# Performance work log

Measured on AMD Instinct MI355X. Metric: run time of the kernel, lower is better.

The kernel has to match this reference:

```python
import jax, jax.numpy as jnp
import numpy as np

B, TV, TH, F, H, D = 16, 128, 64, 512, 512, 256


def setup_inputs() -> dict:
    key = jax.random.key(0)
    ks = jax.random.split(key, 6)
    return {
        "v": jax.random.normal(ks[0], (B, TV, F), dtype=jnp.float32),
        "h": jax.random.normal(ks[1], (B, TH, H), dtype=jnp.float32),
        "W": jax.random.normal(ks[2], (F, D), dtype=jnp.float32) * 0.05,
        "U": jax.random.normal(ks[3], (H, D), dtype=jnp.float32) * 0.05,
        "b": jax.random.normal(ks[4], (D,), dtype=jnp.float32) * 0.05,
        "w": jax.random.normal(ks[5], (D, 1), dtype=jnp.float32) * 0.05,
    }


def reference(v, h, W, U, b, w):
    # v: [B, Tv, F] video features; h: [B, Th, H] decoder hidden states
    Wv = jnp.einsum("btf,fd->btd", v, W)      # [B, Tv, D]
    Uh = jnp.einsum("bsh,hd->bsd", h, U)      # [B, Th, D]
    # Broadcast add -> [B, Th, Tv, D], tanh nonlinearity (additive attention)
    f = jnp.tanh(Uh[:, :, None, :] + Wv[:, None, :, :] + b)
    q = jnp.einsum("bstd,d->bst", f, w[:, 0])  # scores [B, Th, Tv]
    beta = jax.nn.softmax(q, axis=-1)           # softmax over Tv (axis -2 of q[..., None])
    u = jnp.einsum("bst,btf->bsf", beta, v)    # context [B, Th, F]
    return u
```

## Files before the change

### kernel.cpp

```cpp
#include <hip/hip_runtime.h>
#include <hip/hip_bf16.h>

#define BB 16
#define TV 128
#define TH 64
#define FF 512
#define HH 512
#define DD 256

#define LOG2E2 2.8853900817779268f

typedef __attribute__((ext_vector_type(8))) short bf16x8;
typedef __attribute__((ext_vector_type(4))) float f32x4;

__device__ __forceinline__ float fast_exp2(float x) {
#if __has_builtin(__builtin_amdgcn_exp2f)
  return __builtin_amdgcn_exp2f(x);
#else
  return __expf(x * 0.6931471805599453f);
#endif
}
__device__ __forceinline__ float fast_rcp(float x) {
#if __has_builtin(__builtin_amdgcn_rcpf)
  return __builtin_amdgcn_rcpf(x);
#else
  return 1.0f / x;
#endif
}
__device__ __forceinline__ unsigned short f2bf(float x) {
  union { float f; unsigned u; } a; a.f = x;
  unsigned r = a.u + 0x7fffu + ((a.u >> 16) & 1u);
  return (unsigned short)(r >> 16);
}

__device__ __forceinline__ bf16x8 cvt8(const float4 x, const float4 y) {
  union { bf16x8 v; unsigned short e[8]; } r;
  r.e[0] = f2bf(x.x); r.e[1] = f2bf(x.y); r.e[2] = f2bf(x.z); r.e[3] = f2bf(x.w);
  r.e[4] = f2bf(y.x); r.e[5] = f2bf(y.y); r.e[6] = f2bf(y.z); r.e[7] = f2bf(y.w);
  return r.v;
}

__global__ __launch_bounds__(256) void convert_wu_kernel(
    const float* __restrict__ W, const float* __restrict__ U,
    unsigned short* __restrict__ WT, unsigned short* __restrict__ UT) {
  int t2 = blockIdx.x * 256 + threadIdx.x;
  const float* S;
  unsigned short* Dt;
  if (t2 < 32768) { S = W; Dt = WT; } else { S = U; Dt = UT; t2 -= 32768; }
  int n = t2 & 255, k4 = t2 >> 8;
  float a0 = S[(k4 * 4 + 0) * 256 + n];
  float a1 = S[(k4 * 4 + 1) * 256 + n];
  float a2 = S[(k4 * 4 + 2) * 256 + n];
  float a3 = S[(k4 * 4 + 3) * 256 + n];
  ushort4 o = make_ushort4(f2bf(a0), f2bf(a1), f2bf(a2), f2bf(a3));
  *(ushort4*)&Dt[(size_t)n * 512 + k4 * 4] = o;
}

__global__ __launch_bounds__(64) void mfma_gemm_kernel(
    const float* __restrict__ Av, const float* __restrict__ Ah,
    const unsigned short* __restrict__ WT, const unsigned short* __restrict__ UT,
    const float* __restrict__ bias, float* __restrict__ EaT,
    float* __restrict__ EuhT) {
  const int bid = blockIdx.x;
  const float* A;
  const unsigned short* BT;
  int mt, nt;
  bool is_wv;
  if (bid < 256) {
    A = Av; BT = WT; is_wv = true;
    mt = bid >> 2; nt = bid & 3;
  } else {
    const int b2 = bid - 256;
    A = Ah; BT = UT; is_wv = false;
    mt = b2 >> 2; nt = b2 & 3;
  }
  const int lane = threadIdx.x & 63;
  const int m0   = mt * 32;
  const int n0   = nt * 64;
  const int r16  = lane & 15;
  const int quad = lane >> 4;

  const float* a0p = A + (size_t)(m0 + r16) * 512 + quad * 8;
  const float* a1p = a0p + 16 * 512;
  const unsigned short* bp0 = BT + (size_t)(n0 + r16) * 512 + quad * 8;
  const unsigned short* bp1 = bp0 + 16 * 512;
  const unsigned short* bp2 = bp0 + 32 * 512;
  const unsigned short* bp3 = bp0 + 48 * 512;

  f32x4 acc[2][4];
#pragma unroll
  for (int i = 0; i < 2; i++)
#pragma unroll
    for (int j = 0; j < 4; j++) acc[i][j] = (f32x4){0.f, 0.f, 0.f, 0.f};

#pragma unroll
  for (int kc = 0; kc < 16; kc++) {
    float4 a0lo = *(const float4*)(a0p + kc * 32);
    float4 a0hi = *(const float4*)(a0p + kc * 32 + 4);
    float4 a1lo = *(const float4*)(a1p + kc * 32);
    float4 a1hi = *(const float4*)(a1p + kc * 32 + 4);
    bf16x8 fa0 = cvt8(a0lo, a0hi);
    bf16x8 fa1 = cvt8(a1lo, a1hi);
    bf16x8 fb0 = *(const bf16x8*)(bp0 + kc * 32);
    bf16x8 fb1 = *(const bf16x8*)(bp1 + kc * 32);
    bf16x8 fb2 = *(const bf16x8*)(bp2 + kc * 32);
    bf16x8 fb3 = *(const bf16x8*)(bp3 + kc * 32);
    acc[0][0] = __builtin_amdgcn_mfma_f32_16x16x32_bf16(fa0, fb0, acc[0][0], 0, 0, 0);
    acc[0][1] = __builtin_amdgcn_mfma_f32_16x16x32_bf16(fa0, fb1, acc[0][1], 0, 0, 0);
    acc[0][2] = __builtin_amdgcn_mfma_f32_16x16x32_bf16(fa0, fb2, acc[0][2], 0, 0, 0);
    acc[0][3] = __builtin_amdgcn_mfma_f32_16x16x32_bf16(fa0, fb3, acc[0][3], 0, 0, 0);
    acc[1][0] = __builtin_amdgcn_mfma_f32_16x16x32_bf16(fa1, fb0, acc[1][0], 0, 0, 0);
    acc[1][1] = __builtin_amdgcn_mfma_f32_16x16x32_bf16(fa1, fb1, acc[1][1], 0, 0, 0);
    acc[1][2] = __builtin_amdgcn_mfma_f32_16x16x32_bf16(fa1, fb2, acc[1][2], 0, 0, 0);
    acc[1][3] = __builtin_amdgcn_mfma_f32_16x16x32_bf16(fa1, fb3, acc[1][3], 0, 0, 0);
  }

  if (is_wv) {
    const int bb = m0 >> 7;
    const int tb = (m0 & 127) + quad * 4;
    float* Wb = EaT + (size_t)bb * 32768;
#pragma unroll
    for (int i = 0; i < 2; i++) {
#pragma unroll
      for (int j = 0; j < 4; j++) {
#pragma unroll
        for (int r = 0; r < 4; r++) {
          Wb[(size_t)(n0 + 16 * j + r16) * 128 + tb + 16 * i + r] =
              fast_exp2(acc[i][j][r] * LOG2E2);
        }
      }
    }
  } else {
    float bj[4];
#pragma unroll
    for (int j = 0; j < 4; j++) bj[j] = bias[n0 + 16 * j + r16];
#pragma unroll
    for (int i = 0; i < 2; i++) {
#pragma unroll
      for (int j = 0; j < 4; j++) {
#pragma unroll
        for (int r = 0; r < 4; r++) {
          const int row = m0 + 16 * i + quad * 4 + r;
          EuhT[(size_t)row * 256 + n0 + 16 * j + r16] =
              fast_exp2((acc[i][j][r] + bj[j]) * LOG2E2);
        }
      }
    }
  }
}

__global__ __launch_bounds__(1024) void attn_fused_kernel(
    const float* __restrict__ EaT, const float* __restrict__ EuhT,
    const float* __restrict__ wg, const float* __restrict__ v,
    float* __restrict__ u) {
  __shared__ float EuhS[4 * 256];
  __shared__ float wS[256];
  __shared__ float pS[4 * 16 * 128];
  __shared__ float bS[4 * 128];
  __shared__ float mW[8];
  __shared__ float sW[8];

  const int tid = threadIdx.x;
  const int bid  = blockIdx.x;
  const int slot = bid >> 3;
  const int b    = (bid & 7) * 2 + (slot >> 4);
  const int sg   = slot & 15;
  const int s0   = sg * 4;

  if (tid < 256) {
    const int row = tid >> 6, q4 = (tid & 63) << 2;
    *(float4*)&EuhS[row * 256 + q4] =
        *(const float4*)&EuhT[(size_t)(b * 64 + s0 + row) * 256 + q4];
  } else if (tid < 320) {
    const int q4 = (tid - 256) << 2;
    *(float4*)&wS[q4] = *(const float4*)&wg[q4];
  }
  __syncthreads();

  {
    const int t4  = tid & 31;
    const int dgf = tid >> 5;
    const float* eab = EaT + (size_t)b * 32768 + (size_t)dgf * 8 * 128 + t4 * 4;

    float eu[4][8];
    float wr[8];
#pragma unroll
    for (int s = 0; s < 4; s++) {
      *(float4*)&eu[s][0] = *(const float4*)&EuhS[s * 256 + dgf * 8];
      *(float4*)&eu[s][4] = *(const float4*)&EuhS[s * 256 + dgf * 8 + 4];
    }
    *(float4*)&wr[0] = *(const float4*)&wS[dgf * 8];
    *(float4*)&wr[4] = *(const float4*)&wS[dgf * 8 + 4];

    f32x4 acc[4];
#pragma unroll
    for (int s = 0; s < 4; s++) acc[s] = (f32x4){0.f, 0.f, 0.f, 0.f};

#pragma unroll
    for (int jp = 0; jp < 4; jp++) {
      float4 e0 = *(const float4*)(eab + (2 * jp + 0) * 128);
      float4 e1 = *(const float4*)(eab + (2 * jp + 1) * 128);
      const float w0 = wr[2 * jp], w1 = wr[2 * jp + 1];
#pragma unroll
      for (int s = 0; s < 4; s++) {
        const float u0 = eu[s][2 * jp], u1 = eu[s][2 * jp + 1];
        float D0, D1, num;
        D0 = fmaf(e0.x, u0, 1.0f); D1 = fmaf(e1.x, u1, 1.0f);
        num = fmaf(w1, D0, w0 * D1);
        acc[s][0] = fmaf(num, fast_rcp(D0 * D1), acc[s][0]);
        D0 = fmaf(e0.y, u0, 1.0f); D1 = fmaf(e1.y, u1, 1.0f);
        num = fmaf(w1, D0, w0 * D1);
        acc[s][1] = fmaf(num, fast_rcp(D0 * D1), acc[s][1]);
        D0 = fmaf(e0.z, u0, 1.0f); D1 = fmaf(e1.z, u1, 1.0f);
        num = fmaf(w1, D0, w0 * D1);
        acc[s][2] = fmaf(num, fast_rcp(D0 * D1), acc[s][2]);
        D0 = fmaf(e0.w, u0, 1.0f); D1 = fmaf(e1.w, u1, 1.0f);
        num = fmaf(w1, D0, w0 * D1);
        acc[s][3] = fmaf(num, fast_rcp(D0 * D1), acc[s][3]);
      }
    }

#pragma unroll
    for (int s = 0; s < 4; s++) {
#pragma unroll
      for (int c = 0; c < 4; c++) acc[s][c] += __shfl_xor(acc[s][c], 32, 64);
    }
    const int wv_ = tid >> 6;
    if ((tid & 63) < 32) {
#pragma unroll
      for (int s = 0; s < 4; s++) {
        float4 o = make_float4(acc[s][0], acc[s][1], acc[s][2], acc[s][3]);
        *(float4*)&pS[(s * 16 + wv_) * 128 + t4 * 4] = o;
      }
    }
  }
  __syncthreads();

  float qv = 0.0f, ev = 0.0f;
  const int wvid = tid >> 6, lane = tid & 63;
  if (tid < 512) {
    const int s_l = tid >> 7, t = tid & 127;
    float ssum = 0.0f;
#pragma unroll
    for (int k = 0; k < 16; k++) ssum += pS[(s_l * 16 + k) * 128 + t];
    qv = ssum * (-LOG2E2);
    float m = qv;
#pragma unroll
    for (int off = 32; off > 0; off >>= 1) m = fmaxf(m, __shfl_xor(m, off, 64));
    if (lane == 0) mW[wvid] = m;
  }
  __syncthreads();
  if (tid < 512) {
    float m = fmaxf(mW[wvid], mW[wvid ^ 1]);
    ev = fast_exp2(qv - m);
    float ssum = ev;
#pragma unroll
    for (int off = 32; off > 0; off >>= 1) ssum += __shfl_xor(ssum, off, 64);
    if (lane == 0) sW[wvid] = ssum;
  }
  __syncthreads();
  if (tid < 512) {
    const int s_l = tid >> 7, t = tid & 127;
    bS[s_l * 128 + t] = ev * fast_rcp(sW[wvid] + sW[wvid ^ 1]);
  }
  __syncthreads();

  const int f  = tid & 511;
  const int th = tid >> 9;
  const float* vb2 = v + (size_t)b * TV * FF + (size_t)th * 64 * FF;
  const float* bsp = &bS[th * 64];
  float a0 = 0.f, a1 = 0.f, a2 = 0.f, a3 = 0.f;
#pragma unroll 4
  for (int tg = 0; tg < 64; tg += 4) {
    float4 b0 = *(const float4*)&bsp[0 * 128 + tg];
    float4 b1 = *(const float4*)&bsp[1 * 128 + tg];
    float4 b2 = *(const float4*)&bsp[2 * 128 + tg];
    float4 b3 = *(const float4*)&bsp[3 * 128 + tg];
    float v0 = vb2[(tg + 0) * 512 + f];
    float v1 = vb2[(tg + 1) * 512 + f];
    float v2 = vb2[(tg + 2) * 512 + f];
    float v3 = vb2[(tg + 3) * 512 + f];
    a0 = fmaf(b0.x, v0, a0); a0 = fmaf(b0.y, v1, a0);
    a0 = fmaf(b0.z, v2, a0); a0 = fmaf(b0.w, v3, a0);
    a1 = fmaf(b1.x, v0, a1); a1 = fmaf(b1.y, v1, a1);
    a1 = fmaf(b1.z, v2, a1); a1 = fmaf(b1.w, v3, a1);
    a2 = fmaf(b2.x, v0, a2); a2 = fmaf(b2.y, v1, a2);
    a2 = fmaf(b2.z, v2, a2); a2 = fmaf(b2.w, v3, a2);
    a3 = fmaf(b3.x, v0, a3); a3 = fmaf(b3.y, v1, a3);
    a3 = fmaf(b3.z, v2, a3); a3 = fmaf(b3.w, v3, a3);
  }
  float* uP = pS;
  uP[(th * 4 + 0) * 512 + f] = a0;
  uP[(th * 4 + 1) * 512 + f] = a1;
  uP[(th * 4 + 2) * 512 + f] = a2;
  uP[(th * 4 + 3) * 512 + f] = a3;
  __syncthreads();
  {
    int oi = tid;
#pragma unroll
    for (int rep = 0; rep < 2; rep++, oi += 1024) {
      const int s = oi >> 9, ff = oi & 511;
      const float val = uP[s * 512 + ff] + uP[(s + 4) * 512 + ff];
      u[(size_t)(b * 64 + s0 + s) * 512 + ff] = val;
    }
  }
}

extern "C" void kernel_launch(void* const* d_in, const int* in_sizes, int n_in,
                              void* d_out, int out_size, void* d_ws, size_t ws_size,
                              hipStream_t stream) {
  const float* v  = (const float*)d_in[0];
  const float* h  = (const float*)d_in[1];
  const float* W  = (const float*)d_in[2];
  const float* U  = (const float*)d_in[3];
  const float* bb = (const float*)d_in[4];
  const float* w  = (const float*)d_in[5];
  float* u = (float*)d_out;

  float* EaT  = (float*)d_ws;
  float* EuhT = EaT + (size_t)2048 * 256;
  unsigned short* WT = (unsigned short*)(EuhT + (size_t)1024 * 256);
  unsigned short* UT = WT + (size_t)256 * 512;

  convert_wu_kernel<<<256, 256, 0, stream>>>(W, U, WT, UT);
  mfma_gemm_kernel<<<384, 64, 0, stream>>>(v, h, WT, UT, bb, EaT, EuhT);
  attn_fused_kernel<<<256, 1024, 0, stream>>>(EaT, EuhT, w, v, u);
}
```

Measured before the change: 91.13 us.

## Split GEMM K dimension across four waves with shared-memory reduction

The projection GEMM kernel now launches 256 threads per block instead of 64. Each of the four waves handles a quarter of the K=512 reduction, and the partial accumulators are summed through shared memory before the exp epilogue. This shortens the serial MFMA/load chain per block and raises the number of waves in flight on a small grid. It adds a 32KB LDS buffer, a block barrier and the reduction traffic.

```diff
diff --git a/kernel.cpp b/kernel.cpp
--- a/kernel.cpp
+++ b/kernel.cpp
@@ -56,11 +56,12 @@
   *(ushort4*)&Dt[(size_t)n * 512 + k4 * 4] = o;
 }
 
-__global__ __launch_bounds__(64) void mfma_gemm_kernel(
+__global__ __launch_bounds__(256) void mfma_gemm_kernel(
     const float* __restrict__ Av, const float* __restrict__ Ah,
     const unsigned short* __restrict__ WT, const unsigned short* __restrict__ UT,
     const float* __restrict__ bias, float* __restrict__ EaT,
     float* __restrict__ EuhT) {
+  __shared__ f32x4 cS[8][4][64];
   const int bid = blockIdx.x;
   const float* A;
   const unsigned short* BT;
@@ -74,15 +75,17 @@
     A = Ah; BT = UT; is_wv = false;
     mt = b2 >> 2; nt = b2 & 3;
   }
-  const int lane = threadIdx.x & 63;
+  const int tid  = threadIdx.x;
+  const int wv   = tid >> 6;
+  const int lane = tid & 63;
   const int m0   = mt * 32;
   const int n0   = nt * 64;
   const int r16  = lane & 15;
   const int quad = lane >> 4;
 
-  const float* a0p = A + (size_t)(m0 + r16) * 512 + quad * 8;
-  const float* a1p = a0p + 16 * 512;
-  const unsigned short* bp0 = BT + (size_t)(n0 + r16) * 512 + quad * 8;
+  const float* ap0 = A + (size_t)(m0 + r16) * 512 + wv * 128 + quad * 8;
+  const float* ap1 = ap0 + 16 * 512;
+  const unsigned short* bp0 = BT + (size_t)(n0 + r16) * 512 + wv * 128 + quad * 8;
   const unsigned short* bp1 = bp0 + 16 * 512;
   const unsigned short* bp2 = bp0 + 32 * 512;
   const unsigned short* bp3 = bp0 + 48 * 512;
@@ -94,11 +97,11 @@
     for (int j = 0; j < 4; j++) acc[i][j] = (f32x4){0.f, 0.f, 0.f, 0.f};
 
 #pragma unroll
-  for (int kc = 0; kc < 16; kc++) {
-    float4 a0lo = *(const float4*)(a0p + kc * 32);
-    float4 a0hi = *(const float4*)(a0p + kc * 32 + 4);
-    float4 a1lo = *(const float4*)(a1p + kc * 32);
-    float4 a1hi = *(const float4*)(a1p + kc * 32 + 4);
+  for (int kc = 0; kc < 4; kc++) {
+    float4 a0lo = *(const float4*)(ap0 + kc * 32);
+    float4 a0hi = *(const float4*)(ap0 + kc * 32 + 4);
+    float4 a1lo = *(const float4*)(ap1 + kc * 32);
+    float4 a1hi = *(const float4*)(ap1 + kc * 32 + 4);
     bf16x8 fa0 = cvt8(a0lo, a0hi);
     bf16x8 fa1 = cvt8(a1lo, a1hi);
     bf16x8 fb0 = *(const bf16x8*)(bp0 + kc * 32);
@@ -115,35 +118,37 @@
     acc[1][3] = __builtin_amdgcn_mfma_f32_16x16x32_bf16(fa1, fb3, acc[1][3], 0, 0, 0);
   }
 
-  if (is_wv) {
-    const int bb = m0 >> 7;
-    const int tb = (m0 & 127) + quad * 4;
-    float* Wb = EaT + (size_t)bb * 32768;
-#pragma unroll
-    for (int i = 0; i < 2; i++) {
-#pragma unroll
-      for (int j = 0; j < 4; j++) {
-#pragma unroll
-        for (int r = 0; r < 4; r++) {
-          Wb[(size_t)(n0 + 16 * j + r16) * 128 + tb + 16 * i + r] =
-              fast_exp2(acc[i][j][r] * LOG2E2);
-        }
+#pragma unroll
+  for (int i = 0; i < 2; i++)
+#pragma unroll
+    for (int j = 0; j < 4; j++) cS[i * 4 + j][wv][lane] = acc[i][j];
+  __syncthreads();
+
+#pragma unroll
+  for (int rep = 0; rep < 2; rep++) {
+    const int slot = wv + rep * 4;
+    const int i = slot >> 2, j = slot & 3;
+    f32x4 s0 = cS[slot][0][lane];
+    f32x4 s1 = cS[slot][1][lane];
+    f32x4 s2 = cS[slot][2][lane];
+    f32x4 s3 = cS[slot][3][lane];
+    f32x4 sum = (s0 + s1) + (s2 + s3);
+    if (is_wv) {
+      const int bb = m0 >> 7;
+      const int tb = (m0 & 127) + 16 * i + quad * 4;
+      float* Wb = EaT + (size_t)bb * 32768;
+#pragma unroll
+      for (int r = 0; r < 4; r++) {
+        Wb[(size_t)(n0 + 16 * j + r16) * 128 + tb + r] =
+            fast_exp2(sum[r] * LOG2E2);
       }
-    }
-  } else {
-    float bj[4];
-#pragma unroll
-    for (int j = 0; j < 4; j++) bj[j] = bias[n0 + 16 * j + r16];
-#pragma unroll
-    for (int i = 0; i < 2; i++) {
-#pragma unroll
-      for (int j = 0; j < 4; j++) {
-#pragma unroll
-        for (int r = 0; r < 4; r++) {
-          const int row = m0 + 16 * i + quad * 4 + r;
-          EuhT[(size_t)row * 256 + n0 + 16 * j + r16] =
-              fast_exp2((acc[i][j][r] + bj[j]) * LOG2E2);
-        }
+    } else {
+      const float bj = bias[n0 + 16 * j + r16];
+#pragma unroll
+      for (int r = 0; r < 4; r++) {
+        const int row = m0 + 16 * i + quad * 4 + r;
+        EuhT[(size_t)row * 256 + n0 + 16 * j + r16] =
+            fast_exp2((sum[r] + bj) * LOG2E2);
       }
     }
   }
@@ -323,6 +328,6 @@
   unsigned short* UT = WT + (size_t)256 * 512;
 
   convert_wu_kernel<<<256, 256, 0, stream>>>(W, U, WT, UT);
-  mfma_gemm_kernel<<<384, 64, 0, stream>>>(v, h, WT, UT, bb, EaT, EuhT);
+  mfma_gemm_kernel<<<384, 256, 0, stream>>>(v, h, WT, UT, bb, EaT, EuhT);
   attn_fused_kernel<<<256, 1024, 0, stream>>>(EaT, EuhT, w, v, u);
 }
```

Result: faster. 88.36 us (-3.0%).
